# Optimization experiments

Measured on AMD Instinct MI355X. Metric: run time of the kernel, lower is better.

Reference implementation:

```python
import jax, jax.numpy as jnp
import numpy as np

IN_C, HID_C, OUT_C = 602, 256, 41
N_SRC0, N_TGT0, N_TGT1 = 256000, 10240, 1024
E0, E1 = 256000, 10240


def setup_inputs() -> dict:
    key = jax.random.key(0)
    ks = jax.random.split(key, 12)
    x = jax.random.normal(ks[0], (N_SRC0, IN_C), dtype=jnp.float32)
    src0 = jax.random.randint(ks[1], (E0,), 0, N_SRC0, dtype=jnp.int32)
    dst0 = jax.random.randint(ks[2], (E0,), 0, N_TGT0, dtype=jnp.int32)
    src1 = jax.random.randint(ks[3], (E1,), 0, N_TGT0, dtype=jnp.int32)
    dst1 = jax.random.randint(ks[4], (E1,), 0, N_TGT1, dtype=jnp.int32)
    s1 = 1.0 / np.sqrt(IN_C)
    s2 = 1.0 / np.sqrt(HID_C)
    Wl1 = jax.random.uniform(ks[5], (IN_C, HID_C), jnp.float32, -s1, s1)
    Wr1 = jax.random.uniform(ks[6], (IN_C, HID_C), jnp.float32, -s1, s1)
    b1 = jnp.zeros((HID_C,), jnp.float32)
    Wl2 = jax.random.uniform(ks[7], (HID_C, OUT_C), jnp.float32, -s2, s2)
    Wr2 = jax.random.uniform(ks[8], (HID_C, OUT_C), jnp.float32, -s2, s2)
    b2 = jnp.zeros((OUT_C,), jnp.float32)
    return {"x": x, "src0": src0, "dst0": dst0, "src1": src1, "dst1": dst1,
            "Wl1": Wl1, "Wr1": Wr1, "b1": b1, "Wl2": Wl2, "Wr2": Wr2, "b2": b2,
            "n_tgt0": N_TGT0, "n_tgt1": N_TGT1}


def _sage_conv(x_src, x_tgt, src, dst, Wl, Wr, b, n_tgt):
    # mean aggregation of source messages per target node (0 for isolated targets)
    msg = x_src[src]                                                   # [E, C]
    ssum = jax.ops.segment_sum(msg, dst, num_segments=n_tgt)           # [n_tgt, C]
    cnt = jax.ops.segment_sum(jnp.ones((src.shape[0], 1), x_src.dtype), dst,
                              num_segments=n_tgt)
    agg = ssum / jnp.maximum(cnt, 1.0)
    return agg @ Wl + x_tgt @ Wr + b


def reference(x, src0, dst0, src1, dst1, Wl1, Wr1, b1, Wl2, Wr2, b2, n_tgt0, n_tgt1):
    # layer 1: bipartite SAGEConv, x_target = x[:n_tgt0]
    h = _sage_conv(x, x[:n_tgt0], src0, dst0, Wl1, Wr1, b1, n_tgt0)
    h = jax.nn.relu(h)  # dropout omitted (eval / deterministic)
    # layer 2
    out = _sage_conv(h, h[:n_tgt1], src1, dst1, Wl2, Wr2, b2, n_tgt1)
    return jax.nn.log_softmax(out, axis=-1)
```

## Files before the change

### kernel.cpp

```cpp
#include <hip/hip_runtime.h>
#include <hip/hip_bf16.h>

#define IN_C   602
#define HID_C  256
#define OUT_C  41
#define N_TGT0 10240
#define N_TGT1 1024
#define E0     256000
#define E1     10240
#define KTOT   1216
#define NWK    (HID_C * KTOT)

typedef unsigned short u16;
typedef __attribute__((ext_vector_type(4))) float f32x4;
typedef __attribute__((ext_vector_type(8))) short bf16x8;

__device__ __forceinline__ u16 f2bf(float v) {
    union { float f; unsigned u; } c; c.f = v;
    unsigned u = c.u;
    u += 0x7fffu + ((u >> 16) & 1u);
    return (u16)(u >> 16);
}
__device__ __forceinline__ float bf2f(u16 v) {
    union { unsigned u; float f; } c; c.u = ((unsigned)v) << 16; return c.f;
}

__global__ __launch_bounds__(256) void build_kernel(
    const int* __restrict__ src0, const int* __restrict__ dst0,
    const int* __restrict__ src1, const int* __restrict__ dst1,
    int* __restrict__ head0, int* __restrict__ next0,
    int* __restrict__ head1, int* __restrict__ next1,
    const float* __restrict__ Wl, const float* __restrict__ Wr, u16* __restrict__ BT)
{
    int id = blockIdx.x * 256 + threadIdx.x;
    if (id < E0) {
        int p = atomicExch(&head0[dst0[id]], id);
        next0[id] = p;
    } else if (id < E0 + E1) {
        int e = id - E0;
        int p = atomicExch(&head1[dst1[e]], e);
        next1[e] = p;
    }
    if (id < NWK) {
        int n = id / KTOT, k = id - n * KTOT;
        float v = 0.f;
        if (k < IN_C)                        v = Wl[(size_t)k * HID_C + n];
        else if (k >= 608 && k < 608 + IN_C) v = Wr[(size_t)(k - 608) * HID_C + n];
        BT[id] = f2bf(v);
    }
}

__global__ __launch_bounds__(256) void agg0_ll(
    const float* __restrict__ x, const int* __restrict__ head,
    const int* __restrict__ next, const int* __restrict__ srcv,
    u16* __restrict__ A)
{
    int t = blockIdx.x * 4 + (threadIdx.x >> 6);
    int lane = threadIdx.x & 63;

    float2 a0 = make_float2(0.f, 0.f), a1 = a0, a2 = a0, a3 = a0, a4 = a0;
    int d = 0;

    int cur = head[t];
    int s   = (cur >= 0) ? srcv[cur] : 0;
    int nxt = (cur >= 0) ? next[cur] : -1;
    while (cur >= 0) {
        const float2* r = (const float2*)(x + (size_t)s * IN_C);
        float2 v0 = r[lane], v1 = r[lane + 64], v2 = r[lane + 128], v3 = r[lane + 192];
        int curN = nxt;
        int sN   = (curN >= 0) ? srcv[curN] : 0;
        int nxtN = (curN >= 0) ? next[curN] : -1;
        a0.x += v0.x; a0.y += v0.y;
        a1.x += v1.x; a1.y += v1.y;
        a2.x += v2.x; a2.y += v2.y;
        a3.x += v3.x; a3.y += v3.y;
        if (lane < 45) {
            float2 v4 = r[lane + 256];
            a4.x += v4.x; a4.y += v4.y;
        }
        ++d;
        cur = curN; s = sN; nxt = nxtN;
    }

    float inv = 1.0f / (float)(d > 1 ? d : 1);
    ushort2* orow = (ushort2*)(A + (size_t)t * KTOT);
    ushort2 o;
    o.x = f2bf(a0.x * inv); o.y = f2bf(a0.y * inv); orow[lane]       = o;
    o.x = f2bf(a1.x * inv); o.y = f2bf(a1.y * inv); orow[lane + 64]  = o;
    o.x = f2bf(a2.x * inv); o.y = f2bf(a2.y * inv); orow[lane + 128] = o;
    o.x = f2bf(a3.x * inv); o.y = f2bf(a3.y * inv); orow[lane + 192] = o;
    if (lane < 45) {
        o.x = f2bf(a4.x * inv); o.y = f2bf(a4.y * inv); orow[lane + 256] = o;
    } else if (lane < 48) {
        o.x = 0; o.y = 0; orow[lane + 256] = o;
    }

    const float2* xt = (const float2*)(x + (size_t)t * IN_C);
    ushort2* orow2 = orow + 304;
    float2 w0 = xt[lane], w1 = xt[lane + 64], w2 = xt[lane + 128], w3 = xt[lane + 192];
    o.x = f2bf(w0.x); o.y = f2bf(w0.y); orow2[lane]       = o;
    o.x = f2bf(w1.x); o.y = f2bf(w1.y); orow2[lane + 64]  = o;
    o.x = f2bf(w2.x); o.y = f2bf(w2.y); orow2[lane + 128] = o;
    o.x = f2bf(w3.x); o.y = f2bf(w3.y); orow2[lane + 192] = o;
    if (lane < 45) {
        float2 w4 = xt[lane + 256];
        o.x = f2bf(w4.x); o.y = f2bf(w4.y); orow2[lane + 256] = o;
    } else if (lane < 48) {
        o.x = 0; o.y = 0; orow2[lane + 256] = o;
    }
}

__global__ __launch_bounds__(256) void gemm1_wave(
    const u16* __restrict__ A, const u16* __restrict__ BT,
    const float* __restrict__ bias, u16* __restrict__ h)
{
    int wid = (blockIdx.x << 2) + (threadIdx.x >> 6);
    int lane = threadIdx.x & 63;
    int wm = wid >> 3, wn = wid & 7;
    int bm = wm * 32, bn = wn * 32;
    int r16 = lane & 15;
    int k8 = (lane >> 4) * 8;

    const u16* pa0 = A  + (size_t)(bm + r16) * KTOT + k8;
    const u16* pa1 = pa0 + 16 * KTOT;
    const u16* pb0 = BT + (size_t)(bn + r16) * KTOT + k8;
    const u16* pb1 = pb0 + 16 * KTOT;

    f32x4 acc[2][2] = {};

    bf16x8 a0 = *(const bf16x8*)(pa0);
    bf16x8 a1 = *(const bf16x8*)(pa1);
    bf16x8 b0 = *(const bf16x8*)(pb0);
    bf16x8 b1 = *(const bf16x8*)(pb1);

    #pragma unroll 2
    for (int k0 = 0; k0 < KTOT; k0 += 32) {
        bf16x8 na0, na1, nb0, nb1;
        if (k0 + 32 < KTOT) {
            na0 = *(const bf16x8*)(pa0 + k0 + 32);
            na1 = *(const bf16x8*)(pa1 + k0 + 32);
            nb0 = *(const bf16x8*)(pb0 + k0 + 32);
            nb1 = *(const bf16x8*)(pb1 + k0 + 32);
        }
        acc[0][0] = __builtin_amdgcn_mfma_f32_16x16x32_bf16(a0, b0, acc[0][0], 0, 0, 0);
        acc[0][1] = __builtin_amdgcn_mfma_f32_16x16x32_bf16(a0, b1, acc[0][1], 0, 0, 0);
        acc[1][0] = __builtin_amdgcn_mfma_f32_16x16x32_bf16(a1, b0, acc[1][0], 0, 0, 0);
        acc[1][1] = __builtin_amdgcn_mfma_f32_16x16x32_bf16(a1, b1, acc[1][1], 0, 0, 0);
        a0 = na0; a1 = na1; b0 = nb0; b1 = nb1;
    }

    int row4 = (lane >> 4) * 4;
    float bia0 = bias[bn + r16];
    float bia1 = bias[bn + 16 + r16];
    #pragma unroll
    for (int fm = 0; fm < 2; ++fm) {
        #pragma unroll
        for (int j = 0; j < 4; ++j) {
            int m = bm + fm * 16 + row4 + j;
            float v0 = acc[fm][0][j] + bia0;
            float v1 = acc[fm][1][j] + bia1;
            h[(size_t)m * HID_C + bn + r16]      = f2bf(v0 > 0.f ? v0 : 0.f);
            h[(size_t)m * HID_C + bn + 16 + r16] = f2bf(v1 > 0.f ? v1 : 0.f);
        }
    }
}

__global__ __launch_bounds__(64) void out_fused(
    const u16* __restrict__ h, const int* __restrict__ head,
    const int* __restrict__ next, const int* __restrict__ srcv,
    const float* __restrict__ Wl, const float* __restrict__ Wr,
    const float* __restrict__ bias, float* __restrict__ out)
{
    __shared__ float arow[HID_C];
    __shared__ float hrow[HID_C];
    int t = blockIdx.x;
    int lane = threadIdx.x;

    float4 acc = make_float4(0.f, 0.f, 0.f, 0.f);
    int d = 0;
    int cur = head[t];
    int s   = (cur >= 0) ? srcv[cur] : 0;
    int nxt = (cur >= 0) ? next[cur] : -1;
    while (cur >= 0) {
        ushort4 v = ((const ushort4*)(h + (size_t)s * HID_C))[lane];
        int curN = nxt;
        int sN   = (curN >= 0) ? srcv[curN] : 0;
        int nxtN = (curN >= 0) ? next[curN] : -1;
        acc.x += bf2f(v.x); acc.y += bf2f(v.y);
        acc.z += bf2f(v.z); acc.w += bf2f(v.w);
        ++d;
        cur = curN; s = sN; nxt = nxtN;
    }
    float inv = 1.0f / (float)(d > 1 ? d : 1);
    ((float4*)arow)[lane] = make_float4(acc.x * inv, acc.y * inv, acc.z * inv, acc.w * inv);
    ushort4 hv = ((const ushort4*)(h + (size_t)t * HID_C))[lane];
    ((float4*)hrow)[lane] = make_float4(bf2f(hv.x), bf2f(hv.y), bf2f(hv.z), bf2f(hv.w));
    __syncthreads();

    float v = 0.f;
    if (lane < OUT_C) {
        v = bias[lane];
        for (int k = 0; k < HID_C; ++k)
            v += arow[k] * Wl[k * OUT_C + lane] + hrow[k] * Wr[k * OUT_C + lane];
    }
    float m = (lane < OUT_C) ? v : -1e30f;
    #pragma unroll
    for (int off = 32; off; off >>= 1) m = fmaxf(m, __shfl_xor(m, off));
    float ex = (lane < OUT_C) ? expf(v - m) : 0.f;
    float sum = ex;
    #pragma unroll
    for (int off = 32; off; off >>= 1) sum += __shfl_xor(sum, off);
    float lse = m + logf(sum);
    if (lane < OUT_C) out[(size_t)t * OUT_C + lane] = v - lse;
}


extern "C" void kernel_launch(void* const* d_in, const int* in_sizes, int n_in,
                              void* d_out, int out_size, void* d_ws, size_t ws_size,
                              hipStream_t stream) {
    const float* x    = (const float*)d_in[0];
    const int*   src0 = (const int*)d_in[1];
    const int*   dst0 = (const int*)d_in[2];
    const int*   src1 = (const int*)d_in[3];
    const int*   dst1 = (const int*)d_in[4];
    const float* Wl1  = (const float*)d_in[5];
    const float* Wr1  = (const float*)d_in[6];
    const float* b1   = (const float*)d_in[7];
    const float* Wl2  = (const float*)d_in[8];
    const float* Wr2  = (const float*)d_in[9];
    const float* b2   = (const float*)d_in[10];
    float* out = (float*)d_out;

    char* ws = (char*)d_ws;
    size_t off = 0;
    auto take = [&](size_t bytes) { void* p = ws + off; off += (bytes + 255) & ~(size_t)255; return p; };
    u16* A     = (u16*)take((size_t)N_TGT0 * KTOT * 2);
    u16* BT    = (u16*)take((size_t)HID_C * KTOT * 2);
    u16* h     = (u16*)take((size_t)N_TGT0 * HID_C * 2);
    int* head0 = (int*)take((size_t)(N_TGT0 + N_TGT1) * 4);
    int* head1 = head0 + N_TGT0;
    int* next0 = (int*)take((size_t)E0 * 4);
    int* next1 = (int*)take((size_t)E1 * 4);

    hipMemsetAsync(head0, 0xFF, (size_t)(N_TGT0 + N_TGT1) * sizeof(int), stream);

    build_kernel<<<(NWK + 255) / 256, 256, 0, stream>>>(
        src0, dst0, src1, dst1, head0, next0, head1, next1, Wl1, Wr1, BT);

    agg0_ll<<<N_TGT0 / 4, 256, 0, stream>>>(x, head0, next0, src0, A);

    gemm1_wave<<<640, 256, 0, stream>>>(A, BT, b1, h);

    out_fused<<<N_TGT1, 64, 0, stream>>>(h, head1, next1, src1, Wl2, Wr2, b2, out);
}
```

Before: 216.1 us.

## Stage GEMM tiles through swizzled LDS with async global-to-LDS double buffering

Replaces the per-wave register-streaming GEMM with 64x64 block tiles staged in shared memory using global_load_lds, double-buffered across K steps, with an XOR swizzle to avoid bank conflicts. Four waves share the A and B tiles, so global traffic per output drops. It adds a barrier per K step and relies on the async LDS loads being complete at the barrier.

```diff
diff --git a/kernel.cpp b/kernel.cpp
--- a/kernel.cpp
+++ b/kernel.cpp
@@ -23,6 +23,12 @@
 }
 __device__ __forceinline__ float bf2f(u16 v) {
     union { unsigned u; float f; } c; c.u = ((unsigned)v) << 16; return c.f;
+}
+
+__device__ __forceinline__ void gload16(const void* g, void* l) {
+    __builtin_amdgcn_global_load_lds(
+        (const __attribute__((address_space(1))) void*)g,
+        (__attribute__((address_space(3))) void*)l, 16, 0, 0);
 }
 
 __global__ __launch_bounds__(256) void build_kernel(
@@ -110,57 +116,86 @@
     }
 }
 
-__global__ __launch_bounds__(256) void gemm1_wave(
+#define GBM 64
+#define GBN 64
+#define GBK 64
+#define GNIT (KTOT / GBK)
+
+__global__ __launch_bounds__(256) void gemm1_tile(
     const u16* __restrict__ A, const u16* __restrict__ BT,
     const float* __restrict__ bias, u16* __restrict__ h)
 {
-    int wid = (blockIdx.x << 2) + (threadIdx.x >> 6);
-    int lane = threadIdx.x & 63;
-    int wm = wid >> 3, wn = wid & 7;
-    int bm = wm * 32, bn = wn * 32;
+    __shared__ __align__(16) u16 As[2][GBM * GBK];
+    __shared__ __align__(16) u16 Bs[2][GBN * GBK];
+    int tid = threadIdx.x;
+    int w = tid >> 6, lane = tid & 63;
+    int d = blockIdx.x;
+    int ni = (d >> 3) & 3;
+    int mi = (d & 7) + ((d >> 5) << 3);
+    int bm = mi * GBM, bn = ni * GBN;
+
     int r16 = lane & 15;
-    int k8 = (lane >> 4) * 8;
-
-    const u16* pa0 = A  + (size_t)(bm + r16) * KTOT + k8;
-    const u16* pa1 = pa0 + 16 * KTOT;
-    const u16* pb0 = BT + (size_t)(bn + r16) * KTOT + k8;
-    const u16* pb1 = pb0 + 16 * KTOT;
+    int g = lane >> 4;
+    int wm2 = w >> 1, wn2 = w & 1;
+
+    int srow = lane >> 3;
+    int sslot = (lane & 7) ^ srow;
+    const u16* gA0 = A  + (size_t)(bm + w * 16 + srow) * KTOT + sslot * 8;
+    const u16* gA1 = gA0 + (size_t)8 * KTOT;
+    const u16* gB0 = BT + (size_t)(bn + w * 16 + srow) * KTOT + sslot * 8;
+    const u16* gB1 = gB0 + (size_t)8 * KTOT;
+
+    int xr = r16 & 7;
+    int rowA0 = wm2 * 32 + r16;
+    int rowB0 = wn2 * 32 + r16;
 
     f32x4 acc[2][2] = {};
 
-    bf16x8 a0 = *(const bf16x8*)(pa0);
-    bf16x8 a1 = *(const bf16x8*)(pa1);
-    bf16x8 b0 = *(const bf16x8*)(pb0);
-    bf16x8 b1 = *(const bf16x8*)(pb1);
-
-    #pragma unroll 2
-    for (int k0 = 0; k0 < KTOT; k0 += 32) {
-        bf16x8 na0, na1, nb0, nb1;
-        if (k0 + 32 < KTOT) {
-            na0 = *(const bf16x8*)(pa0 + k0 + 32);
-            na1 = *(const bf16x8*)(pa1 + k0 + 32);
-            nb0 = *(const bf16x8*)(pb0 + k0 + 32);
-            nb1 = *(const bf16x8*)(pb1 + k0 + 32);
+    auto stage = [&](int buf, int k0) {
+        u16* dA = &As[buf][w * 1024];
+        u16* dB = &Bs[buf][w * 1024];
+        gload16(gA0 + k0, dA);
+        gload16(gA1 + k0, dA + 512);
+        gload16(gB0 + k0, dB);
+        gload16(gB1 + k0, dB + 512);
+    };
+
+    stage(0, 0);
+    __syncthreads();
+
+    int cur = 0;
+    for (int it = 0; it < GNIT; ++it) {
+        if (it + 1 < GNIT) stage(cur ^ 1, (it + 1) * GBK);
+
+        #pragma unroll
+        for (int ks = 0; ks < 2; ++ks) {
+            int sl = ((ks << 2) + g);
+            bf16x8 a0 = *(const bf16x8*)(&As[cur][rowA0 * 64 + ((sl ^ xr) << 3)]);
+            bf16x8 a1 = *(const bf16x8*)(&As[cur][(rowA0 + 16) * 64 + ((sl ^ xr) << 3)]);
+            bf16x8 b0 = *(const bf16x8*)(&Bs[cur][rowB0 * 64 + ((sl ^ xr) << 3)]);
+            bf16x8 b1 = *(const bf16x8*)(&Bs[cur][(rowB0 + 16) * 64 + ((sl ^ xr) << 3)]);
+            acc[0][0] = __builtin_amdgcn_mfma_f32_16x16x32_bf16(a0, b0, acc[0][0], 0, 0, 0);
+            acc[0][1] = __builtin_amdgcn_mfma_f32_16x16x32_bf16(a0, b1, acc[0][1], 0, 0, 0);
+            acc[1][0] = __builtin_amdgcn_mfma_f32_16x16x32_bf16(a1, b0, acc[1][0], 0, 0, 0);
+            acc[1][1] = __builtin_amdgcn_mfma_f32_16x16x32_bf16(a1, b1, acc[1][1], 0, 0, 0);
         }
-        acc[0][0] = __builtin_amdgcn_mfma_f32_16x16x32_bf16(a0, b0, acc[0][0], 0, 0, 0);
-        acc[0][1] = __builtin_amdgcn_mfma_f32_16x16x32_bf16(a0, b1, acc[0][1], 0, 0, 0);
-        acc[1][0] = __builtin_amdgcn_mfma_f32_16x16x32_bf16(a1, b0, acc[1][0], 0, 0, 0);
-        acc[1][1] = __builtin_amdgcn_mfma_f32_16x16x32_bf16(a1, b1, acc[1][1], 0, 0, 0);
-        a0 = na0; a1 = na1; b0 = nb0; b1 = nb1;
-    }
-
-    int row4 = (lane >> 4) * 4;
-    float bia0 = bias[bn + r16];
-    float bia1 = bias[bn + 16 + r16];
+        __syncthreads();
+        cur ^= 1;
+    }
+
+    int row4 = g * 4;
     #pragma unroll
-    for (int fm = 0; fm < 2; ++fm) {
+    for (int fn = 0; fn < 2; ++fn) {
+        int n = bn + wn2 * 32 + fn * 16 + r16;
+        float b = bias[n];
         #pragma unroll
-        for (int j = 0; j < 4; ++j) {
-            int m = bm + fm * 16 + row4 + j;
-            float v0 = acc[fm][0][j] + bia0;
-            float v1 = acc[fm][1][j] + bia1;
-            h[(size_t)m * HID_C + bn + r16]      = f2bf(v0 > 0.f ? v0 : 0.f);
-            h[(size_t)m * HID_C + bn + 16 + r16] = f2bf(v1 > 0.f ? v1 : 0.f);
+        for (int fm = 0; fm < 2; ++fm) {
+            #pragma unroll
+            for (int j = 0; j < 4; ++j) {
+                int m = bm + wm2 * 32 + fm * 16 + row4 + j;
+                float v = acc[fm][fn][j] + b;
+                h[(size_t)m * HID_C + n] = f2bf(v > 0.f ? v : 0.f);
+            }
         }
     }
 }
@@ -249,7 +284,7 @@
 
     agg0_ll<<<N_TGT0 / 4, 256, 0, stream>>>(x, head0, next0, src0, A);
 
-    gemm1_wave<<<640, 256, 0, stream>>>(A, BT, b1, h);
+    gemm1_tile<<<640, 256, 0, stream>>>(A, BT, b1, h);
 
     out_fused<<<N_TGT1, 64, 0, stream>>>(h, head1, next1, src1, Wl2, Wr2, b2, out);
 }
```

After: 186.0 us. -13.9%, faster.
